# Kernel optimization log

Hardware: AMD Instinct MI355X
Metric: run time of the kernel (lower is better)

The kernel has to match this reference:

```python
import jax, jax.numpy as jnp
import numpy as np

NUM_EXPERTS = 8
TOP_K = 2


def setup_inputs() -> dict:
    key = jax.random.key(0)
    k1, k2, k3, k4, k5 = jax.random.split(key, 5)
    B, S, D, H, E = 4, 2048, 1024, 2048, NUM_EXPERTS
    scale_d = 1.0 / np.sqrt(D)
    scale_h = 1.0 / np.sqrt(H)
    return {
        "hidden_states": jax.random.normal(k1, (B, S, D), dtype=jnp.float32),
        "router_w": jax.random.normal(k2, (E, D), dtype=jnp.float32) * scale_d,
        "gate_w": jax.random.normal(k3, (E, H, D), dtype=jnp.float32) * scale_d,
        "up_w": jax.random.normal(k4, (E, H, D), dtype=jnp.float32) * scale_d,
        "down_w": jax.random.normal(k5, (E, D, H), dtype=jnp.float32) * scale_h,
    }


def reference(hidden_states, router_w, gate_w, up_w, down_w):
    B, S, D = hidden_states.shape
    E = router_w.shape[0]
    x = hidden_states.reshape(-1, D)  # [T, D]
    T = x.shape[0]

    # Router: softmax over experts, top-k, renormalize selected probs.
    router_logits = x @ router_w.T                      # [T, E]
    routing_probs = jax.nn.softmax(router_logits, axis=-1)
    top_k_probs, top_k_idx = jax.lax.top_k(routing_probs, TOP_K)  # [T, K]
    top_k_probs = top_k_probs / jnp.sum(top_k_probs, axis=-1, keepdims=True)

    # Combine weights: combine[t, e] = sum_k p[t, k] * (idx[t, k] == e)
    t_idx = jnp.arange(T)[:, None]                      # [T, 1]
    combine = jnp.zeros((T, E), dtype=x.dtype).at[t_idx, top_k_idx].add(top_k_probs)

    # Dense expert compute weighted by combine (fixed small loop over experts).
    out = jnp.zeros_like(x)
    for e in range(E):
        gate = x @ gate_w[e].T                          # [T, H]
        up = x @ up_w[e].T                              # [T, H]
        expert_out = (jax.nn.silu(gate) * up) @ down_w[e].T  # [T, D]
        out = out + expert_out * combine[:, e:e + 1]
    return out.reshape(B, S, D)
```

## Files before the change

### kernel.cpp

```cpp
#include <hip/hip_runtime.h>

typedef __attribute__((ext_vector_type(4))) float f32x4;
typedef __attribute__((ext_vector_type(8))) short bf16x8;

constexpr int TOK = 8192;
constexpr int DD  = 1024;
constexpr int HH  = 2048;
constexpr int NE  = 8;
constexpr int SB  = TOK / 256;


__device__ __forceinline__ unsigned short f2bf(float f) {
    union { float f; unsigned u; } v; v.f = f;
    unsigned r = v.u + 0x7fffu + ((v.u >> 16) & 1u);
    return (unsigned short)(r >> 16);
}

__device__ __forceinline__ void gl2lds16(const void* g, void* l) {
    __builtin_amdgcn_global_load_lds(
        (const __attribute__((address_space(1))) unsigned int*)g,
        (__attribute__((address_space(3))) unsigned int*)l, 16, 0, 0);
}

__global__ __launch_bounds__(256) void k_router(
    const float* __restrict__ x, const float* __restrict__ rw,
    int* __restrict__ topk_idx, float* __restrict__ topk_prob,
    unsigned short* __restrict__ x_bf)
{
    int wave = threadIdx.x >> 6;
    int lane = threadIdx.x & 63;
    int t = blockIdx.x * 4 + wave;

    const float4* xr = (const float4*)(x + (size_t)t * DD);
    float4 xv[4];
#pragma unroll
    for (int i = 0; i < 4; i++) xv[i] = xr[lane + 64 * i];

#pragma unroll
    for (int i = 0; i < 4; i++) {
        ushort4 u4 = make_ushort4(f2bf(xv[i].x), f2bf(xv[i].y),
                                  f2bf(xv[i].z), f2bf(xv[i].w));
        *(ushort4*)(x_bf + (size_t)t * DD + (lane + 64 * i) * 4) = u4;
    }

    float acc[NE];
#pragma unroll
    for (int e = 0; e < NE; e++) {
        const float4* wr = (const float4*)(rw + (size_t)e * DD);
        float s = 0.f;
#pragma unroll
        for (int i = 0; i < 4; i++) {
            float4 w = wr[lane + 64 * i];
            s += xv[i].x * w.x + xv[i].y * w.y + xv[i].z * w.z + xv[i].w * w.w;
        }
        acc[e] = s;
    }
#pragma unroll
    for (int e = 0; e < NE; e++) {
        float s = acc[e];
        for (int m = 32; m >= 1; m >>= 1) s += __shfl_xor(s, m);
        acc[e] = s;
    }
    if (lane == 0) {
        int b0 = 0; float l0 = acc[0];
#pragma unroll
        for (int e = 1; e < NE; e++) if (acc[e] > l0) { l0 = acc[e]; b0 = e; }
        int b1 = -1; float l1 = -3.0e38f;
#pragma unroll
        for (int e = 0; e < NE; e++) if (e != b0 && acc[e] > l1) { l1 = acc[e]; b1 = e; }
        float p0 = 1.f / (1.f + __expf(l1 - l0));
        float p1 = 1.f - p0;
        topk_idx[t * 2 + 0] = b0;  topk_idx[t * 2 + 1] = b1;
        topk_prob[t * 2 + 0] = p0; topk_prob[t * 2 + 1] = p1;
    }
}

__global__ __launch_bounds__(256) void k_hist(
    const int* __restrict__ topk_idx, int* __restrict__ blk_hist)
{
    __shared__ int h[NE];
    if (threadIdx.x < NE) h[threadIdx.x] = 0;
    __syncthreads();
    int t = blockIdx.x * 256 + threadIdx.x;
    atomicAdd(&h[topk_idx[t * 2 + 0]], 1);
    atomicAdd(&h[topk_idx[t * 2 + 1]], 1);
    __syncthreads();
    if (threadIdx.x < NE)
        blk_hist[blockIdx.x * NE + threadIdx.x] = h[threadIdx.x];
}

__global__ void k_scan2(const int* __restrict__ blk_hist, int* __restrict__ offsets,
                        int* __restrict__ base)
{
    __shared__ int totals[NE];
    int e = threadIdx.x;
    if (e < NE) {
        int run = 0;
        for (int b = 0; b < SB; b++) {
            base[b * NE + e] = run;
            run += blk_hist[b * NE + e];
        }
        totals[e] = run;
    }
    __syncthreads();
    if (threadIdx.x == 0) {
        int s = 0;
        for (int ee = 0; ee < NE; ee++) { offsets[ee] = s; s += totals[ee]; }
        offsets[NE] = s;
    }
    __syncthreads();
    if (e < NE) {
        int o = offsets[e];
        for (int b = 0; b < SB; b++) base[b * NE + e] += o;
    }
}

__global__ __launch_bounds__(256) void k_scatter2(
    const int* __restrict__ topk_idx, const float* __restrict__ topk_prob,
    const int* __restrict__ base,
    int* __restrict__ token_list, float* __restrict__ prob_list,
    int* __restrict__ slot)
{
    __shared__ int cur[NE];
    if (threadIdx.x < NE) cur[threadIdx.x] = base[blockIdx.x * NE + threadIdx.x];
    __syncthreads();
    int t = blockIdx.x * 256 + threadIdx.x;
#pragma unroll
    for (int k = 0; k < 2; k++) {
        int e = topk_idx[t * 2 + k];
        int pos = atomicAdd(&cur[e], 1);
        token_list[pos] = t;
        prob_list[pos] = topk_prob[t * 2 + k];
        slot[t * 2 + k] = pos;
    }
}

__global__ __launch_bounds__(256) void k_cvt_all(
    const float* __restrict__ gw, const float* __restrict__ uw,
    const float* __restrict__ dw,
    unsigned short* __restrict__ gwb, unsigned short* __restrict__ uwb,
    unsigned short* __restrict__ dwb)
{
    constexpr int SEG = NE * HH * DD / 8;
    int i = blockIdx.x * blockDim.x + threadIdx.x;
    int stride = gridDim.x * blockDim.x;
    for (; i < 3 * SEG; i += stride) {
        const float* in; unsigned short* out; int j = i;
        if (j < SEG)            { in = gw; out = gwb; }
        else if (j < 2 * SEG)   { in = uw; out = uwb; j -= SEG; }
        else                    { in = dw; out = dwb; j -= 2 * SEG; }
        const float4* p = (const float4*)(in + (size_t)j * 8);
        float4 a = p[0], b = p[1];
        uint4 v;
        v.x = (unsigned)f2bf(a.x) | ((unsigned)f2bf(a.y) << 16);
        v.y = (unsigned)f2bf(a.z) | ((unsigned)f2bf(a.w) << 16);
        v.z = (unsigned)f2bf(b.x) | ((unsigned)f2bf(b.y) << 16);
        v.w = (unsigned)f2bf(b.z) | ((unsigned)f2bf(b.w) << 16);
        *(uint4*)(out + (size_t)j * 8) = v;
    }
}

__global__ __launch_bounds__(512) void k_gateup_v3(
    const unsigned short* __restrict__ xb,
    const unsigned short* __restrict__ gwb,
    const unsigned short* __restrict__ uwb,
    const int* __restrict__ offsets,
    const int* __restrict__ token_list,
    unsigned short* __restrict__ act)
{
    extern __shared__ char lds[];

    const int bid = blockIdx.x;
    const int e   = bid & 7;
    const int r   = bid >> 3;
    const int m   = r >> 4;
    const int n   = r & 15;
    const int off = offsets[e];
    const int n_e = offsets[e + 1] - off;
    const int m0  = m * 128;
    if (m0 >= n_e) return;
    const int n0g = n * 128;

    const int tid = threadIdx.x, lane = tid & 63, wid = tid >> 6;
    const int wm = wid >> 2, wn = wid & 3;
    const int l8 = lane >> 3;
    const int colb = ((lane & 7) * 16) ^ (l8 << 4);

    const char* src[6];
    unsigned ldsoff[6];
#pragma unroll
    for (int i = 0; i < 6; i++) {
        int c = wid * 6 + i;
        if (c < 16) {
            int tr = c * 8 + l8;
            int rg = m0 + tr; if (rg > n_e - 1) rg = n_e - 1;
            int tok = token_list[off + rg];
            src[i] = (const char*)xb + (size_t)tok * (DD * 2) + colb;
            ldsoff[i] = c * 1024u;
        } else {
            int cb = c - 16;
            int tr = cb * 8 + l8;
            int wr = tr >> 6, w = tr & 63;
            const unsigned short* W = (w < 32) ? gwb : uwb;
            int wcol = n0g + wr * 32 + (w & 31);
            src[i] = (const char*)W + ((size_t)e * HH + wcol) * (DD * 2) + colb;
            ldsoff[i] = 16384u + cb * 1024u;
        }
    }

    f32x4 acc[4][4] = {};

#define GU_STAGE(T) do { char* b_ = lds + ((T) % 3) * 49152u; \
    _Pragma("unroll") for (int i_ = 0; i_ < 6; i_++) \
        gl2lds16(src[i_] + (T) * 128, b_ + ldsoff[i_]); } while (0)

    GU_STAGE(0);
    GU_STAGE(1);
    asm volatile("s_waitcnt vmcnt(6)" ::: "memory");
    __builtin_amdgcn_s_barrier();
    asm volatile("" ::: "memory");

    constexpr int NT = (DD * 2) / 128;
    for (int t = 0; t < NT; ++t) {
        if (t + 2 < NT) GU_STAGE(t + 2);
        const char* La = lds + (t % 3) * 49152u;
        const char* Lb = La + 16384;
        __builtin_amdgcn_s_setprio(1);
#pragma unroll
        for (int kk = 0; kk < 2; kk++) {
            const int kb = kk * 64 + (lane >> 4) * 16;
            bf16x8 af[4], bfr[4];
#pragma unroll
            for (int mi = 0; mi < 4; mi++) {
                int row = wm * 64 + mi * 16 + (lane & 15);
                af[mi] = *(const bf16x8*)(La + row * 128 + (kb ^ ((row & 7) << 4)));
            }
#pragma unroll
            for (int nj = 0; nj < 4; nj++) {
                int br = wn * 64 + nj * 16 + (lane & 15);
                bfr[nj] = *(const bf16x8*)(Lb + br * 128 + (kb ^ ((br & 7) << 4)));
            }
#pragma unroll
            for (int mi = 0; mi < 4; mi++)
#pragma unroll
                for (int nj = 0; nj < 4; nj++)
                    acc[mi][nj] = __builtin_amdgcn_mfma_f32_16x16x32_bf16(af[mi], bfr[nj], acc[mi][nj], 0, 0, 0);
        }
        __builtin_amdgcn_s_setprio(0);
        if (t + 2 < NT)      asm volatile("s_waitcnt vmcnt(6)" ::: "memory");
        else if (t + 1 < NT) asm volatile("s_waitcnt vmcnt(0)" ::: "memory");
        __builtin_amdgcn_s_barrier();
        asm volatile("" ::: "memory");
    }
#undef GU_STAGE

#pragma unroll
    for (int mi = 0; mi < 4; mi++) {
#pragma unroll
        for (int r2 = 0; r2 < 4; r2++) {
            int row = wm * 64 + mi * 16 + (lane >> 4) * 4 + r2;
            int rg = m0 + row;
            if (rg >= n_e) continue;
            size_t rowbase = (size_t)(off + rg) * HH + n0g + wn * 32;
#pragma unroll
            for (int nj = 0; nj < 2; nj++) {
                float gg = acc[mi][nj][r2];
                float uu = acc[mi][nj + 2][r2];
                float sv = gg / (1.f + __expf(-gg)) * uu;
                act[rowbase + nj * 16 + (lane & 15)] = f2bf(sv);
            }
        }
    }
}

__global__ __launch_bounds__(256) void k_down_v5(
    const unsigned short* __restrict__ act,
    const unsigned short* __restrict__ dwb,
    const int* __restrict__ offsets,
    unsigned short* __restrict__ y)
{
    __shared__ char lds[32768];

    const int bid = blockIdx.x;
    const int e   = bid & 7;
    const int rem = bid >> 3;
    const int n   = rem >> 6;
    const int m   = rem & 63;
    const int off = offsets[e];
    const int n_e = offsets[e + 1] - off;
    const int m0  = m * 128;
    if (m0 >= n_e) return;
    const int n0  = n * 128;

    const int tid = threadIdx.x, lane = tid & 63, wid = tid >> 6;
    const int wm = wid >> 1, wn = wid & 1;
    const int l8 = lane >> 3, l15 = lane & 15;
    const int colb = ((lane & 7) * 16) ^ (l8 << 4);

    const char* src[8];
#pragma unroll
    for (int i = 0; i < 8; i++) {
        int c = wid * 8 + i;
        if (c < 16) {
            int rg = m0 + c * 8 + l8; if (rg > n_e - 1) rg = n_e - 1;
            src[i] = (const char*)act + (size_t)(off + rg) * (HH * 2) + colb;
        } else {
            int tr = (c - 16) * 8 + l8;
            src[i] = (const char*)dwb + ((size_t)e * DD + n0 + tr) * (HH * 2) + colb;
        }
    }

    f32x4 acc[4][4] = {};

    constexpr int NT = (HH * 2) / 128;
    for (int t = 0; t < NT; ++t) {
        __syncthreads();
#pragma unroll
        for (int i = 0; i < 8; i++)
            gl2lds16(src[i] + t * 128, lds + (wid * 8 + i) * 1024);
        __syncthreads();
#pragma unroll
        for (int kk = 0; kk < 2; kk++) {
            const int kb = kk * 64 + (lane >> 4) * 16;
            bf16x8 af[4], bfr[4];
#pragma unroll
            for (int mi = 0; mi < 4; mi++) {
                int row = wm * 64 + mi * 16 + l15;
                af[mi] = *(const bf16x8*)(lds + row * 128 + (kb ^ ((row & 7) << 4)));
            }
#pragma unroll
            for (int nj = 0; nj < 4; nj++) {
                int br = wn * 64 + nj * 16 + l15;
                bfr[nj] = *(const bf16x8*)(lds + 16384 + br * 128 + (kb ^ ((br & 7) << 4)));
            }
#pragma unroll
            for (int mi = 0; mi < 4; mi++)
#pragma unroll
                for (int nj = 0; nj < 4; nj++)
                    acc[mi][nj] = __builtin_amdgcn_mfma_f32_16x16x32_bf16(
                        af[mi], bfr[nj], acc[mi][nj], 0, 0, 0);
        }
    }

#pragma unroll
    for (int mi = 0; mi < 4; mi++) {
#pragma unroll
        for (int r2 = 0; r2 < 4; r2++) {
            int row = wm * 64 + mi * 16 + (lane >> 4) * 4 + r2;
            int rg = m0 + row;
            if (rg >= n_e) continue;
            size_t ybase = (size_t)(off + rg) * DD + n0 + wn * 64;
#pragma unroll
            for (int nj = 0; nj < 4; nj++)
                y[ybase + nj * 16 + l15] = f2bf(acc[mi][nj][r2]);
        }
    }
}

__global__ __launch_bounds__(256) void k_combine(
    const unsigned short* __restrict__ y,
    const int* __restrict__ slot,
    const float* __restrict__ topk_prob,
    float* __restrict__ out)
{
    int t = blockIdx.x * 2 + (threadIdx.x >> 7);
    int i = threadIdx.x & 127;
    int s0 = slot[t * 2 + 0], s1 = slot[t * 2 + 1];
    float p0 = topk_prob[t * 2 + 0], p1 = topk_prob[t * 2 + 1];
    bf16x8 a = *(const bf16x8*)(y + (size_t)s0 * DD + i * 8);
    bf16x8 b = *(const bf16x8*)(y + (size_t)s1 * DD + i * 8);
    float o[8];
#pragma unroll
    for (int j = 0; j < 8; j++) {
        union { unsigned u; float f; } va, vb;
        va.u = ((unsigned)(unsigned short)a[j]) << 16;
        vb.u = ((unsigned)(unsigned short)b[j]) << 16;
        o[j] = p0 * va.f + p1 * vb.f;
    }
    float4* op = (float4*)(out + (size_t)t * DD + i * 8);
    op[0] = make_float4(o[0], o[1], o[2], o[3]);
    op[1] = make_float4(o[4], o[5], o[6], o[7]);
}

extern "C" void kernel_launch(void* const* d_in, const int* in_sizes, int n_in,
                              void* d_out, int out_size, void* d_ws, size_t ws_size,
                              hipStream_t stream) {
    const float* x  = (const float*)d_in[0];
    const float* rw = (const float*)d_in[1];
    const float* gw = (const float*)d_in[2];
    const float* uw = (const float*)d_in[3];
    const float* dw = (const float*)d_in[4];
    float* out = (float*)d_out;

    char* ws = (char*)d_ws;
    int*   topk_idx   = (int*)(ws + 0);
    float* topk_prob  = (float*)(ws + 65536);
    int*   offsets    = (int*)(ws + 131072);
    int*   blk_hist   = (int*)(ws + 131136);
    int*   base       = (int*)(ws + 133184);
    int*   token_list = (int*)(ws + 137216);
    float* prob_list  = (float*)(ws + 202752);
    int*   slot       = (int*)(ws + 268288);

    unsigned short* x_bf  = (unsigned short*)(ws + 524288);
    unsigned short* y     = (unsigned short*)(ws + 524288);
    unsigned short* gw_bf = (unsigned short*)(ws + 17301504);
    unsigned short* uw_bf = (unsigned short*)(ws + 50855936);
    unsigned short* dw_bf = (unsigned short*)(ws + 84410368);
    unsigned short* act   = (unsigned short*)(ws + 117964800);

    k_router<<<TOK / 4, 256, 0, stream>>>(x, rw, topk_idx, topk_prob, x_bf);
    k_hist<<<SB, 256, 0, stream>>>(topk_idx, blk_hist);
    k_scan2<<<1, 64, 0, stream>>>(blk_hist, offsets, base);
    k_scatter2<<<SB, 256, 0, stream>>>(topk_idx, topk_prob, base,
                                       token_list, prob_list, slot);

    k_cvt_all<<<2048, 256, 0, stream>>>(gw, uw, dw, gw_bf, uw_bf, dw_bf);

    k_gateup_v3<<<8192, 512, 147456, stream>>>(x_bf, gw_bf, uw_bf, offsets,
                                               token_list, act);
    k_down_v5<<<4096, 256, 0, stream>>>(act, dw_bf, offsets, y);

    k_combine<<<TOK / 2, 256, 0, stream>>>(y, slot, topk_prob, out);
}
```

Baseline: 374.1 us.

## Pre-gather routed tokens, split weight conversion, and simplify gate/up GEMM tiling

Adds a gather kernel that copies routed token rows into a contiguous per-expert buffer, so the gate/up GEMM loads A rows without indirection. The gate/up kernel moves from 512-thread blocks with a 3-stage async LDS pipeline and 128-column tiles to 256-thread blocks with 64-column tiles, a single 32 KB LDS buffer and synchronous load/barrier per K step. The down-weight conversion is split out and run after gate/up so workspace buffers can alias. The risk is that dropping the multi-stage pipeline exposes memory latency, and the extra gather pass adds traffic.

Result: slower. 406.4 us (+8.6%).

```diff
diff --git a/kernel.cpp b/kernel.cpp
--- a/kernel.cpp
+++ b/kernel.cpp
@@ -135,20 +135,31 @@
     }
 }
 
-__global__ __launch_bounds__(256) void k_cvt_all(
+__global__ __launch_bounds__(256) void k_gather(
+    const unsigned short* __restrict__ x_bf,
+    const int* __restrict__ token_list,
+    unsigned short* __restrict__ xg)
+{
+    int row = blockIdx.x * 8 + (threadIdx.x >> 5);
+    int th  = threadIdx.x & 31;
+    int tok = token_list[row];
+    const uint4* s = (const uint4*)(x_bf + (size_t)tok * DD);
+    uint4* d = (uint4*)(xg + (size_t)row * DD);
+#pragma unroll
+    for (int i = 0; i < 4; i++) d[th + 32 * i] = s[th + 32 * i];
+}
+
+__global__ __launch_bounds__(256) void k_cvt_gu(
     const float* __restrict__ gw, const float* __restrict__ uw,
-    const float* __restrict__ dw,
-    unsigned short* __restrict__ gwb, unsigned short* __restrict__ uwb,
-    unsigned short* __restrict__ dwb)
+    unsigned short* __restrict__ gwb, unsigned short* __restrict__ uwb)
 {
     constexpr int SEG = NE * HH * DD / 8;
     int i = blockIdx.x * blockDim.x + threadIdx.x;
     int stride = gridDim.x * blockDim.x;
-    for (; i < 3 * SEG; i += stride) {
+    for (; i < 2 * SEG; i += stride) {
         const float* in; unsigned short* out; int j = i;
-        if (j < SEG)            { in = gw; out = gwb; }
-        else if (j < 2 * SEG)   { in = uw; out = uwb; j -= SEG; }
-        else                    { in = dw; out = dwb; j -= 2 * SEG; }
+        if (j < SEG) { in = gw; out = gwb; }
+        else         { in = uw; out = uwb; j -= SEG; }
         const float4* p = (const float4*)(in + (size_t)j * 8);
         float4 a = p[0], b = p[1];
         uint4 v;
@@ -160,99 +171,96 @@
     }
 }
 
-__global__ __launch_bounds__(512) void k_gateup_v3(
-    const unsigned short* __restrict__ xb,
+__global__ __launch_bounds__(256) void k_cvt_dw(
+    const float* __restrict__ dw, unsigned short* __restrict__ dwb)
+{
+    constexpr int SEG = NE * DD * HH / 8;
+    int i = blockIdx.x * blockDim.x + threadIdx.x;
+    int stride = gridDim.x * blockDim.x;
+    for (; i < SEG; i += stride) {
+        const float4* p = (const float4*)(dw + (size_t)i * 8);
+        float4 a = p[0], b = p[1];
+        uint4 v;
+        v.x = (unsigned)f2bf(a.x) | ((unsigned)f2bf(a.y) << 16);
+        v.y = (unsigned)f2bf(a.z) | ((unsigned)f2bf(a.w) << 16);
+        v.z = (unsigned)f2bf(b.x) | ((unsigned)f2bf(b.y) << 16);
+        v.w = (unsigned)f2bf(b.z) | ((unsigned)f2bf(b.w) << 16);
+        *(uint4*)(dwb + (size_t)i * 8) = v;
+    }
+}
+
+__global__ __launch_bounds__(256) void k_gateup_v9(
+    const unsigned short* __restrict__ xg,
     const unsigned short* __restrict__ gwb,
     const unsigned short* __restrict__ uwb,
     const int* __restrict__ offsets,
-    const int* __restrict__ token_list,
     unsigned short* __restrict__ act)
 {
-    extern __shared__ char lds[];
+    __shared__ char lds[32768];
 
     const int bid = blockIdx.x;
     const int e   = bid & 7;
-    const int r   = bid >> 3;
-    const int m   = r >> 4;
-    const int n   = r & 15;
+    const int rem = bid >> 3;
+    const int n   = rem >> 6;
+    const int m   = rem & 63;
     const int off = offsets[e];
     const int n_e = offsets[e + 1] - off;
     const int m0  = m * 128;
     if (m0 >= n_e) return;
-    const int n0g = n * 128;
+    const int n0  = n * 64;
 
     const int tid = threadIdx.x, lane = tid & 63, wid = tid >> 6;
-    const int wm = wid >> 2, wn = wid & 3;
-    const int l8 = lane >> 3;
+    const int wm = wid >> 1, wn = wid & 1;
+    const int l8 = lane >> 3, l15 = lane & 15;
     const int colb = ((lane & 7) * 16) ^ (l8 << 4);
 
-    const char* src[6];
-    unsigned ldsoff[6];
-#pragma unroll
-    for (int i = 0; i < 6; i++) {
-        int c = wid * 6 + i;
+    const char* src[8];
+#pragma unroll
+    for (int i = 0; i < 8; i++) {
+        int c = wid * 8 + i;
         if (c < 16) {
-            int tr = c * 8 + l8;
-            int rg = m0 + tr; if (rg > n_e - 1) rg = n_e - 1;
-            int tok = token_list[off + rg];
-            src[i] = (const char*)xb + (size_t)tok * (DD * 2) + colb;
-            ldsoff[i] = c * 1024u;
+            int rg = m0 + c * 8 + l8; if (rg > n_e - 1) rg = n_e - 1;
+            src[i] = (const char*)xg + (size_t)(off + rg) * (DD * 2) + colb;
         } else {
-            int cb = c - 16;
-            int tr = cb * 8 + l8;
-            int wr = tr >> 6, w = tr & 63;
-            const unsigned short* W = (w < 32) ? gwb : uwb;
-            int wcol = n0g + wr * 32 + (w & 31);
+            int tr = (c - 16) * 8 + l8;
+            int h = tr >> 6, j = tr & 63;
+            const unsigned short* W = (j < 32) ? gwb : uwb;
+            int wcol = n0 + h * 32 + (j & 31);
             src[i] = (const char*)W + ((size_t)e * HH + wcol) * (DD * 2) + colb;
-            ldsoff[i] = 16384u + cb * 1024u;
         }
     }
 
     f32x4 acc[4][4] = {};
-
-#define GU_STAGE(T) do { char* b_ = lds + ((T) % 3) * 49152u; \
-    _Pragma("unroll") for (int i_ = 0; i_ < 6; i_++) \
-        gl2lds16(src[i_] + (T) * 128, b_ + ldsoff[i_]); } while (0)
-
-    GU_STAGE(0);
-    GU_STAGE(1);
-    asm volatile("s_waitcnt vmcnt(6)" ::: "memory");
-    __builtin_amdgcn_s_barrier();
-    asm volatile("" ::: "memory");
 
     constexpr int NT = (DD * 2) / 128;
     for (int t = 0; t < NT; ++t) {
-        if (t + 2 < NT) GU_STAGE(t + 2);
-        const char* La = lds + (t % 3) * 49152u;
-        const char* Lb = La + 16384;
-        __builtin_amdgcn_s_setprio(1);
+        __syncthreads();
+#pragma unroll
+        for (int i = 0; i < 8; i++)
+            gl2lds16(src[i] + t * 128, lds + (wid * 8 + i) * 1024);
+        __syncthreads();
 #pragma unroll
         for (int kk = 0; kk < 2; kk++) {
             const int kb = kk * 64 + (lane >> 4) * 16;
             bf16x8 af[4], bfr[4];
 #pragma unroll
             for (int mi = 0; mi < 4; mi++) {
-                int row = wm * 64 + mi * 16 + (lane & 15);
-                af[mi] = *(const bf16x8*)(La + row * 128 + (kb ^ ((row & 7) << 4)));
+                int row = wm * 64 + mi * 16 + l15;
+                af[mi] = *(const bf16x8*)(lds + row * 128 + (kb ^ ((row & 7) << 4)));
             }
 #pragma unroll
             for (int nj = 0; nj < 4; nj++) {
-                int br = wn * 64 + nj * 16 + (lane & 15);
-                bfr[nj] = *(const bf16x8*)(Lb + br * 128 + (kb ^ ((br & 7) << 4)));
+                int br = wn * 64 + nj * 16 + l15;
+                bfr[nj] = *(const bf16x8*)(lds + 16384 + br * 128 + (kb ^ ((br & 7) << 4)));
             }
 #pragma unroll
             for (int mi = 0; mi < 4; mi++)
 #pragma unroll
                 for (int nj = 0; nj < 4; nj++)
-                    acc[mi][nj] = __builtin_amdgcn_mfma_f32_16x16x32_bf16(af[mi], bfr[nj], acc[mi][nj], 0, 0, 0);
-        }
-        __builtin_amdgcn_s_setprio(0);
-        if (t + 2 < NT)      asm volatile("s_waitcnt vmcnt(6)" ::: "memory");
-        else if (t + 1 < NT) asm volatile("s_waitcnt vmcnt(0)" ::: "memory");
-        __builtin_amdgcn_s_barrier();
-        asm volatile("" ::: "memory");
-    }
-#undef GU_STAGE
+                    acc[mi][nj] = __builtin_amdgcn_mfma_f32_16x16x32_bf16(
+                        af[mi], bfr[nj], acc[mi][nj], 0, 0, 0);
+        }
+    }
 
 #pragma unroll
     for (int mi = 0; mi < 4; mi++) {
@@ -261,13 +269,13 @@
             int row = wm * 64 + mi * 16 + (lane >> 4) * 4 + r2;
             int rg = m0 + row;
             if (rg >= n_e) continue;
-            size_t rowbase = (size_t)(off + rg) * HH + n0g + wn * 32;
+            size_t rowbase = (size_t)(off + rg) * HH + n0 + wn * 32;
 #pragma unroll
             for (int nj = 0; nj < 2; nj++) {
                 float gg = acc[mi][nj][r2];
                 float uu = acc[mi][nj + 2][r2];
                 float sv = gg / (1.f + __expf(-gg)) * uu;
-                act[rowbase + nj * 16 + (lane & 15)] = f2bf(sv);
+                act[rowbase + nj * 16 + l15] = f2bf(sv);
             }
         }
     }
@@ -399,26 +407,30 @@
     int*   blk_hist   = (int*)(ws + 131136);
     int*   base       = (int*)(ws + 133184);
     int*   token_list = (int*)(ws + 137216);
-    float* prob_list  = (float*)(ws + 202752);
+    float* prob_list  = (float*)(ws + 202752);  (void)prob_list;
     int*   slot       = (int*)(ws + 268288);
 
-    unsigned short* x_bf  = (unsigned short*)(ws + 524288);
-    unsigned short* y     = (unsigned short*)(ws + 524288);
-    unsigned short* gw_bf = (unsigned short*)(ws + 17301504);
-    unsigned short* uw_bf = (unsigned short*)(ws + 50855936);
-    unsigned short* dw_bf = (unsigned short*)(ws + 84410368);
-    unsigned short* act   = (unsigned short*)(ws + 117964800);
+    unsigned short* xg    = (unsigned short*)(ws + 524288);
+    unsigned short* dw_bf = (unsigned short*)(ws + 524288);
+    unsigned short* gw_bf = (unsigned short*)(ws + 34078720);
+    unsigned short* y     = (unsigned short*)(ws + 34078720);
+    unsigned short* uw_bf = (unsigned short*)(ws + 67633152);
+    unsigned short* x_bf  = (unsigned short*)(ws + 101187584);
+    unsigned short* act   = (unsigned short*)(ws + 101187584);
 
     k_router<<<TOK / 4, 256, 0, stream>>>(x, rw, topk_idx, topk_prob, x_bf);
     k_hist<<<SB, 256, 0, stream>>>(topk_idx, blk_hist);
     k_scan2<<<1, 64, 0, stream>>>(blk_hist, offsets, base);
     k_scatter2<<<SB, 256, 0, stream>>>(topk_idx, topk_prob, base,
-                                       token_list, prob_list, slot);
-
-    k_cvt_all<<<2048, 256, 0, stream>>>(gw, uw, dw, gw_bf, uw_bf, dw_bf);
-
-    k_gateup_v3<<<8192, 512, 147456, stream>>>(x_bf, gw_bf, uw_bf, offsets,
-                                               token_list, act);
+                                       token_list, (float*)(ws + 202752), slot);
+    k_gather<<<2 * TOK / 8, 256, 0, stream>>>(x_bf, token_list, xg);
+
+    k_cvt_gu<<<2048, 256, 0, stream>>>(gw, uw, gw_bf, uw_bf);
+
+    k_gateup_v9<<<16384, 256, 0, stream>>>(xg, gw_bf, uw_bf, offsets, act);
+
+    k_cvt_dw<<<2048, 256, 0, stream>>>(dw, dw_bf);
+
     k_down_v5<<<4096, 256, 0, stream>>>(act, dw_bf, offsets, y);
 
     k_combine<<<TOK / 2, 256, 0, stream>>>(y, slot, topk_prob, out);
```
